# Kernel tuning notes

Measured on AMD Instinct MI355X. Metric: run time of the kernel, lower is better.

## Reference

```python
import jax, jax.numpy as jnp
import numpy as np

D_MODEL = 256
KSIZE = 16
EPS = 1e-5


def conv1d(x, w, b):
    # x: [B, C, N], w: [O, C, K], SAME padding over node axis
    y = jax.lax.conv_general_dilated(x, w, window_strides=(1,), padding='SAME',
                                     dimension_numbers=('NCH', 'OIH', 'NCH'))
    return y + b[None, :, None]


def layernorm(x, g, b):
    mu = jnp.mean(x, axis=-1, keepdims=True)
    var = jnp.mean(jnp.square(x - mu), axis=-1, keepdims=True)
    return (x - mu) * jax.lax.rsqrt(var + EPS) * g + b


def setup_inputs() -> dict:
    key = jax.random.key(0)
    ks = jax.random.split(key, 16)
    B, N, d, K = 4, 2048, D_MODEL, KSIZE
    conv_scale = 1.0 / np.sqrt(d * K)
    lin_scale = 1.0 / np.sqrt(d)
    return {
        'src': jax.random.normal(ks[0], (B, N, d), jnp.float32),
        'x_lst': jnp.zeros((B, N, N), jnp.float32),
        'adj': jax.random.randint(ks[1], (B, N, N), 0, 2, jnp.int32),
        'dis': jax.random.uniform(ks[2], (B, N, N), jnp.float32),
        'Wq': jax.random.normal(ks[3], (d, d, K), jnp.float32) * conv_scale,
        'bq': jnp.zeros((d,), jnp.float32),
        'Wk': jax.random.normal(ks[4], (d, d, K), jnp.float32) * conv_scale,
        'bk': jnp.zeros((d,), jnp.float32),
        'Wv': jax.random.normal(ks[5], (d, d, K), jnp.float32) * conv_scale,
        'bv': jnp.zeros((d,), jnp.float32),
        'W1': jax.random.normal(ks[6], (d, d), jnp.float32) * lin_scale,
        'b1': jnp.zeros((d,), jnp.float32),
        'W2': jax.random.normal(ks[7], (d, d), jnp.float32) * lin_scale,
        'b2': jnp.zeros((d,), jnp.float32),
        'W3': jax.random.normal(ks[8], (d, d), jnp.float32) * lin_scale,
        'b3': jnp.zeros((d,), jnp.float32),
        'g1': jnp.ones((d,), jnp.float32),
        'be1': jnp.zeros((d,), jnp.float32),
        'g2': jnp.ones((d,), jnp.float32),
        'be2': jnp.zeros((d,), jnp.float32),
    }


def reference(src, x_lst, adj, dis, Wq, bq, Wk, bk, Wv, bv,
              W1, b1, W2, b2, W3, b3, g1, be1, g2, be2):
    # ---- _ga_block: transpose to channel-major, graph attention ----
    x = jnp.swapaxes(src, -2, -1)                      # [B, d, N]
    q = conv1d(x, Wq, bq)                              # [B, d, N]
    k = conv1d(x, Wk, bk)
    v = conv1d(x, Wv, bv)
    scale = 1.0 / jnp.sqrt(jnp.asarray(D_MODEL, src.dtype))
    scores = jnp.einsum('bdn,bdm->bnm', q, k) * scale  # [B, N, N]
    scores = scores - dis                              # distance bias
    scores = jnp.where(adj > 0, scores, jnp.asarray(-1e9, scores.dtype))
    attn = jax.nn.softmax(scores, axis=-1)             # [B, N, N]
    x_lst_new = x_lst + attn                           # accumulated attention state
    out = jnp.einsum('bnm,bdm->bdn', attn, v)          # [B, d, N]
    x1 = jnp.swapaxes(out, -2, -1)                     # [B, N, d] (dropout = identity in eval)
    # ---- residual + norm1 ----
    h = layernorm(src + x1, g1, be1)
    # ---- 3-layer LeakyReLU MLP + residual + norm2 ----
    m = jax.nn.leaky_relu(h @ W1.T + b1)
    m = jax.nn.leaky_relu(m @ W2.T + b2)
    m = m @ W3.T + b3
    h = layernorm(h + m, g2, be2)
    return h, x_lst_new
```

## Files before the change

kernel.cpp:

```cpp
#include <hip/hip_runtime.h>
#include <stdint.h>

typedef _Float16 h16;
typedef _Float16 h4v __attribute__((ext_vector_type(4)));
typedef _Float16 h8v __attribute__((ext_vector_type(8)));
typedef float    f4v __attribute__((ext_vector_type(4)));
typedef int      i4v __attribute__((ext_vector_type(4)));

#define NBATCH 4
#define NNODE  2048
#define DM     256
#define NPAD   2063
#define QKELEM 2097152
#define PARTN  (8192 * 256)

__device__ __forceinline__ void async16(const void* g, void* l) {
#if __has_builtin(__builtin_amdgcn_global_load_lds)
  __builtin_amdgcn_global_load_lds((__attribute__((address_space(1))) void*)g,
                                   (__attribute__((address_space(3))) void*)l, 16, 0, 0);
#else
  *(f4v*)l = *(const f4v*)g;
#endif
}

#define BARRIER() do { asm volatile("" ::: "memory"); __builtin_amdgcn_s_barrier(); asm volatile("" ::: "memory"); } while (0)
#define MFMA16 __builtin_amdgcn_mfma_f32_16x16x32_f16

__device__ __forceinline__ void gemm_tile(
    const h16* Abase, int astride,
    const h16* Bbase, int bstride,
    h16* As, h16* Bs, f4v acc[4][4], int kiters)
{
  const int tid  = threadIdx.x;
  const int lane = tid & 63;
  const int wv   = tid >> 6;
  const int srow = tid >> 2;
  const int sch  = ((tid & 3) ^ ((tid >> 3) & 3)) * 8;
  const h16* gA0 = Abase + (long)srow * astride + sch;
  const h16* gA1 = Abase + (long)(srow + 64) * astride + sch;
  const h16* gB0 = Bbase + (long)srow * bstride + sch;
  const h16* gB1 = Bbase + (long)(srow + 64) * bstride + sch;
  h16* lA0 = As + tid * 8;
  h16* lA1 = As + 2048 + tid * 8;
  h16* lB0 = Bs + tid * 8;
  h16* lB1 = Bs + 2048 + tid * 8;
  const int swz = ((lane & 15) >> 1) & 3;
  const int qq  = ((lane >> 4) ^ swz) * 8;
  const int amr = ((wv & 1) * 64 + (lane & 15)) * 32 + qq;
  const int bnr = ((wv >> 1) * 64 + (lane & 15)) * 32 + qq;

  for (int kt = 0; kt < kiters; ++kt) {
    const int k0 = kt * 32;
    __syncthreads();
    async16(gA0 + k0, lA0);
    async16(gA1 + k0, lA1);
    async16(gB0 + k0, lB0);
    async16(gB1 + k0, lB1);
    asm volatile("s_waitcnt vmcnt(0)" ::: "memory");
    __syncthreads();
    h8v af[4], bf[4];
#pragma unroll
    for (int i = 0; i < 4; ++i) af[i] = *(const h8v*)(As + amr + i * 512);
#pragma unroll
    for (int j = 0; j < 4; ++j) bf[j] = *(const h8v*)(Bs + bnr + j * 512);
#pragma unroll
    for (int i = 0; i < 4; ++i)
#pragma unroll
      for (int j = 0; j < 4; ++j)
        acc[i][j] = MFMA16(af[i], bf[j], acc[i][j], 0, 0, 0);
  }
}

__device__ __forceinline__ void zero_acc(f4v acc[4][4]) {
#pragma unroll
  for (int i = 0; i < 4; ++i)
#pragma unroll
    for (int j = 0; j < 4; ++j) {
      f4v z = {0.f, 0.f, 0.f, 0.f};
      acc[i][j] = z;
    }
}

#define NSRC_BLK 8252
__global__ __launch_bounds__(256) void prep_all_kernel(
    const float* __restrict__ src,
    const float* __restrict__ Wq, const float* __restrict__ Wk, const float* __restrict__ Wv,
    const float* __restrict__ W1, const float* __restrict__ W2, const float* __restrict__ W3,
    h16* __restrict__ Xpad, h16* __restrict__ Wt, h16* __restrict__ Wl)
{
  __shared__ float plds[16][257];
  const int bi = blockIdx.x, tid = threadIdx.x;
  if (bi < NSRC_BLK) {
    int idx = bi * 256 + tid;
    int c = idx & 255;
    int row = idx >> 8;
    int b = row / NPAD;
    int n = row - b * NPAD;
    float v = 0.f;
    int ns = n - 7;
    if (ns >= 0 && ns < NNODE) v = src[((long)b * NNODE + ns) * DM + c];
    Xpad[idx] = (h16)v;
  } else if (bi < NSRC_BLK + 768) {
    const int q = bi - NSRC_BLK;
    const int w = q >> 8, o = q & 255;
    const float* W = (w == 0) ? Wq : (w == 1) ? Wk : Wv;
    const float* base = W + (long)o * 4096;
    f4v r0 = *(const f4v*)(base + tid * 16);
    f4v r1 = *(const f4v*)(base + tid * 16 + 4);
    f4v r2 = *(const f4v*)(base + tid * 16 + 8);
    f4v r3 = *(const f4v*)(base + tid * 16 + 12);
#pragma unroll
    for (int k = 0; k < 4; ++k) {
      plds[k][tid] = r0[k]; plds[4 + k][tid] = r1[k];
      plds[8 + k][tid] = r2[k]; plds[12 + k][tid] = r3[k];
    }
    __syncthreads();
    const int t = tid >> 4, c0 = (tid & 15) * 16;
    h16* out = Wt + ((long)(w * 256 + o)) * 4096 + t * 256 + c0;
    h8v o0, o1;
#pragma unroll
    for (int k = 0; k < 8; ++k) { o0[k] = (h16)plds[t][c0 + k]; o1[k] = (h16)plds[t][c0 + 8 + k]; }
    *(h8v*)out = o0;
    *(h8v*)(out + 8) = o1;
  } else {
    int idx = (bi - NSRC_BLK - 768) * 256 + tid;
    int w = idx >> 16;
    int rem = idx & 65535;
    const float* W = (w == 0) ? W1 : (w == 1) ? W2 : W3;
    Wl[idx] = (h16)W[rem];
  }
}

__global__ __launch_bounds__(512) void conv_gemm256_kernel(
    const h16* __restrict__ Xpad, const h16* __restrict__ Wt,
    h16* __restrict__ Qp, h16* __restrict__ Kp, h16* __restrict__ Vp)
{
  __shared__ __align__(16) h16 As[32768];
  __shared__ __align__(16) h16 Bs[32768];
  const int tid  = threadIdx.x;
  const int lane = tid & 63, wv = tid >> 6;
  const int mt = blockIdx.x, w = blockIdx.y, ks = blockIdx.z;
  const int m0 = mt * 256;
  const int b  = m0 >> 11, n0 = m0 & 2047;

  const int rh = tid >> 3;
  const int cs = (((tid & 7) ^ ((tid >> 3) & 7)) << 3);
  const h16* AgT = Xpad + ((long)(b * NPAD + n0) << 8) + ((long)ks << 11) + (long)rh * 256 + cs;
  const h16* BgT = Wt + ((long)w << 20) + ((long)ks << 11) + (long)rh * 4096 + cs;
  h16* lA = As + tid * 8;
  h16* lB = Bs + tid * 8;

  auto stageA = [&](int kt, int half) {
    h16* d = lA + ((kt & 1) << 14) + (half << 13);
    const h16* g = AgT + half * (128 * 256) + kt * 64;
    async16(g, d);
    async16(g + 64 * 256, d + 4096);
  };
  auto stageB = [&](int kt, int half) {
    h16* d = lB + ((kt & 1) << 14) + (half << 13);
    const h16* g = BgT + half * (128 * 4096) + kt * 64;
    async16(g, d);
    async16(g + 64 * 4096, d + 4096);
  };

  const int wr = wv >> 2, wc = wv & 3;
  const int e0 = (((lane >> 4) ^ (lane & 7)) << 3);
  const int e1 = e0 ^ 32;
  const h16* pA0 = As + (wr * 128 + (lane & 15)) * 64 + e0;
  const h16* pA1 = pA0 + (e1 - e0);
  const h16* pB0 = Bs + (wc * 64 + (lane & 15)) * 64 + e0;
  const h16* pB1 = pB0 + (e1 - e0);

  f4v acc[8][4];
#pragma unroll
  for (int i = 0; i < 8; ++i)
#pragma unroll
    for (int j = 0; j < 4; ++j) { f4v z = {0.f, 0.f, 0.f, 0.f}; acc[i][j] = z; }

  stageA(0, 0); stageA(0, 1); stageB(0, 0); stageB(0, 1); stageA(1, 0);
  asm volatile("s_waitcnt vmcnt(2)" ::: "memory");
  BARRIER();

#pragma unroll 1
  for (int kt = 0; kt < 32; ++kt) {
    const int sb = (kt & 1) << 14;
    h8v ar[4][2], bL[2][2], bR[2][2];
#pragma unroll
    for (int i = 0; i < 4; ++i) {
      ar[i][0] = *(const h8v*)(pA0 + sb + i * 1024);
      ar[i][1] = *(const h8v*)(pA1 + sb + i * 1024);
    }
#pragma unroll
    for (int j = 0; j < 2; ++j) {
      bL[j][0] = *(const h8v*)(pB0 + sb + j * 1024);
      bL[j][1] = *(const h8v*)(pB1 + sb + j * 1024);
    }
    if (kt < 31) stageA(kt + 1, 1);
    BARRIER();
    __builtin_amdgcn_s_setprio(1);
#pragma unroll
    for (int i = 0; i < 4; ++i)
#pragma unroll
      for (int j = 0; j < 2; ++j) {
        acc[i][j] = MFMA16(ar[i][0], bL[j][0], acc[i][j], 0, 0, 0);
        acc[i][j] = MFMA16(ar[i][1], bL[j][1], acc[i][j], 0, 0, 0);
      }
    __builtin_amdgcn_s_setprio(0);
    BARRIER();
#pragma unroll
    for (int j = 0; j < 2; ++j) {
      bR[j][0] = *(const h8v*)(pB0 + sb + (j + 2) * 1024);
      bR[j][1] = *(const h8v*)(pB1 + sb + (j + 2) * 1024);
    }
    if (kt < 31) stageB(kt + 1, 0);
    BARRIER();
    __builtin_amdgcn_s_setprio(1);
#pragma unroll
    for (int i = 0; i < 4; ++i)
#pragma unroll
      for (int j = 0; j < 2; ++j) {
        acc[i][j + 2] = MFMA16(ar[i][0], bR[j][0], acc[i][j + 2], 0, 0, 0);
        acc[i][j + 2] = MFMA16(ar[i][1], bR[j][1], acc[i][j + 2], 0, 0, 0);
      }
    __builtin_amdgcn_s_setprio(0);
    BARRIER();
#pragma unroll
    for (int i = 0; i < 4; ++i) {
      ar[i][0] = *(const h8v*)(pA0 + sb + (i + 4) * 1024);
      ar[i][1] = *(const h8v*)(pA1 + sb + (i + 4) * 1024);
    }
    if (kt < 31) stageB(kt + 1, 1);
    BARRIER();
    __builtin_amdgcn_s_setprio(1);
#pragma unroll
    for (int i = 0; i < 4; ++i)
#pragma unroll
      for (int j = 0; j < 2; ++j) {
        acc[i + 4][j + 2] = MFMA16(ar[i][0], bR[j][0], acc[i + 4][j + 2], 0, 0, 0);
        acc[i + 4][j + 2] = MFMA16(ar[i][1], bR[j][1], acc[i + 4][j + 2], 0, 0, 0);
      }
    __builtin_amdgcn_s_setprio(0);
    BARRIER();
#pragma unroll
    for (int j = 0; j < 2; ++j) {
      bL[j][0] = *(const h8v*)(pB0 + sb + j * 1024);
      bL[j][1] = *(const h8v*)(pB1 + sb + j * 1024);
    }
    if (kt < 30) {
      stageA(kt + 2, 0);
      asm volatile("s_waitcnt vmcnt(2)" ::: "memory");
    } else if (kt == 30) {
      asm volatile("s_waitcnt vmcnt(0)" ::: "memory");
    }
    BARRIER();
    __builtin_amdgcn_s_setprio(1);
#pragma unroll
    for (int i = 0; i < 4; ++i)
#pragma unroll
      for (int j = 0; j < 2; ++j) {
        acc[i + 4][j] = MFMA16(ar[i][0], bL[j][0], acc[i + 4][j], 0, 0, 0);
        acc[i + 4][j] = MFMA16(ar[i][1], bL[j][1], acc[i + 4][j], 0, 0, 0);
      }
    __builtin_amdgcn_s_setprio(0);
    BARRIER();
  }

  h16* dst = ((w == 0) ? Qp : (w == 1) ? Kp : Vp) + (long)ks * QKELEM;
  const int rb = (lane >> 4) * 4;
  const int cb = wc * 64 + (lane & 15);
  const int mrow0 = m0 + wr * 128;
#pragma unroll
  for (int i = 0; i < 8; ++i)
#pragma unroll
    for (int j = 0; j < 4; ++j) {
      const int gc = cb + j * 16;
#pragma unroll
      for (int e = 0; e < 4; ++e) {
        const int gr = mrow0 + i * 16 + rb + e;
        dst[(long)gr * 256 + gc] = (h16)acc[i][j][e];
      }
    }
}

__global__ __launch_bounds__(256) void conv_reduce_kernel(
    const h16* __restrict__ Qp, const h16* __restrict__ Kp, const h16* __restrict__ Vp,
    const float* __restrict__ bq, const float* __restrict__ bk, const float* __restrict__ bv,
    h16* __restrict__ Qb, h16* __restrict__ Kb, h16* __restrict__ Vt)
{
  __shared__ float T[64][65];
  const int bi = blockIdx.x, tid = threadIdx.x;
  if (bi < 2048) {
    const long gid = (long)bi * 256 + tid;
    const int which = gid >= (QKELEM / 8);
    const long e = (gid - (long)which * (QKELEM / 8)) * 8;
    const h16* P = which ? Kp : Qp;
    const float* bias = which ? bk : bq;
    h8v p0 = *(const h8v*)(P + e);
    h8v p1 = *(const h8v*)(P + QKELEM + e);
    const int c0 = (int)(e & 255);
    h8v o;
#pragma unroll
    for (int k = 0; k < 8; ++k) o[k] = (h16)((float)p0[k] + (float)p1[k] + bias[c0 + k]);
    *(h8v*)((which ? Kb : Qb) + e) = o;
  } else {
    const int q = bi - 2048;
    const int mt = q >> 2, ct = q & 3;
    const int m0 = mt * 64, c0 = ct * 64;
    const int b = m0 >> 11, n0 = m0 & 2047;
    const int rr = tid >> 3, cc = (tid & 7) * 8;
#pragma unroll
    for (int p = 0; p < 2; ++p) {
      const int r = p * 32 + rr;
      const long so = (long)(m0 + r) * 256 + c0 + cc;
      h8v p0 = *(const h8v*)(Vp + so);
      h8v p1 = *(const h8v*)(Vp + QKELEM + so);
#pragma unroll
      for (int e = 0; e < 8; ++e) T[r][cc + e] = (float)p0[e] + (float)p1[e];
    }
    __syncthreads();
#pragma unroll
    for (int p = 0; p < 2; ++p) {
      const int d = p * 32 + rr;
      const float bias_v = bv[c0 + d];
      h8v o;
#pragma unroll
      for (int e = 0; e < 8; ++e) o[e] = (h16)(T[cc + e][d] + bias_v);
      *(h8v*)(Vt + ((long)(b * 256 + c0 + d)) * 2048 + n0 + cc) = o;
    }
  }
}

__global__ __launch_bounds__(256) void scores_gemm_kernel(
    const h16* __restrict__ Q, const h16* __restrict__ Km, h16* __restrict__ Sh)
{
  __shared__ __align__(16) h16 As[4096];
  __shared__ __align__(16) h16 Bs[4096];
  const int nt = blockIdx.x, mt = blockIdx.y, b = blockIdx.z;
  const h16* Abase = Q + ((long)b * NNODE + nt * 128) * 256;
  const h16* Bbase = Km + ((long)b * NNODE + mt * 128) * 256;
  f4v acc[4][4];
  zero_acc(acc);
  gemm_tile(Abase, 256, Bbase, 256, As, Bs, acc, 8);

  const int lane = threadIdx.x & 63, wv = threadIdx.x >> 6;
  const int rbase = (wv & 1) * 64 + (lane >> 4) * 4;
  const int cbase = (wv >> 1) * 64 + (lane & 15);
  h16* Srow = Sh + (long)b * NNODE * NNODE;
#pragma unroll
  for (int i = 0; i < 4; ++i) {
#pragma unroll
    for (int e = 0; e < 4; ++e) {
      const long row = nt * 128 + rbase + i * 16 + e;
#pragma unroll
      for (int j = 0; j < 4; ++j) {
        const int col = mt * 128 + cbase + j * 16;
        Srow[row * 2048 + col] = (h16)(acc[i][j][e] * 0.0625f);
      }
    }
  }
}

__device__ __forceinline__ float wred_max(float v) {
#pragma unroll
  for (int off = 32; off > 0; off >>= 1) v = fmaxf(v, __shfl_xor(v, off, 64));
  return v;
}
__device__ __forceinline__ float wred_sum(float v) {
#pragma unroll
  for (int off = 32; off > 0; off >>= 1) v += __shfl_xor(v, off, 64);
  return v;
}

__global__ __launch_bounds__(256) void softmax_kernel(
    h16* __restrict__ Sh, const float* __restrict__ dis, const int* __restrict__ adj,
    const float* __restrict__ x_lst, float* __restrict__ out_x)
{
  const int r = blockIdx.x;
  const long ro = (long)r * 2048;
  const int tid = threadIdx.x, lane = tid & 63, wv = tid >> 6;
  const int j0 = tid * 8;
  __shared__ float wmax[4], wsum[4];

  h8v sv = *(const h8v*)(Sh + ro + j0);
  f4v d0 = *(const f4v*)(dis + ro + j0);
  f4v d1 = *(const f4v*)(dis + ro + j0 + 4);
  i4v a0 = *(const i4v*)(adj + ro + j0);
  i4v a1 = *(const i4v*)(adj + ro + j0 + 4);

  float s[8];
#pragma unroll
  for (int k = 0; k < 4; ++k) s[k]     = (a0[k] > 0) ? ((float)sv[k]     - d0[k]) : -1e9f;
#pragma unroll
  for (int k = 0; k < 4; ++k) s[k + 4] = (a1[k] > 0) ? ((float)sv[k + 4] - d1[k]) : -1e9f;

  float m = s[0];
#pragma unroll
  for (int k = 1; k < 8; ++k) m = fmaxf(m, s[k]);
  m = wred_max(m);
  if (lane == 0) wmax[wv] = m;
  __syncthreads();
  m = fmaxf(fmaxf(wmax[0], wmax[1]), fmaxf(wmax[2], wmax[3]));

  float p[8], ls = 0.f;
#pragma unroll
  for (int k = 0; k < 8; ++k) { p[k] = __expf(s[k] - m); ls += p[k]; }
  ls = wred_sum(ls);
  if (lane == 0) wsum[wv] = ls;
  __syncthreads();
  const float inv = 1.0f / (wsum[0] + wsum[1] + wsum[2] + wsum[3]);

  f4v x0 = *(const f4v*)(x_lst + ro + j0);
  f4v x1 = *(const f4v*)(x_lst + ro + j0 + 4);
  f4v o0, o1;
  h8v pv;
#pragma unroll
  for (int k = 0; k < 4; ++k) {
    const float a = p[k] * inv, bq = p[k + 4] * inv;
    o0[k] = x0[k] + a; o1[k] = x1[k] + bq;
    pv[k] = (h16)a; pv[k + 4] = (h16)bq;
  }
  *(f4v*)(out_x + ro + j0) = o0;
  *(f4v*)(out_x + ro + j0 + 4) = o1;
  *(h8v*)(Sh + ro + j0) = pv;
}

__global__ __launch_bounds__(256) void av_gemm_kernel(
    const h16* __restrict__ Attn, const h16* __restrict__ Vt, h16* __restrict__ X1p)
{
  __shared__ __align__(16) h16 As[4096];
  __shared__ __align__(16) h16 Bs[4096];
  const int nt = blockIdx.x, b = blockIdx.z;
  const int ct = blockIdx.y & 1, ks = blockIdx.y >> 1;
  const h16* Abase = Attn + ((long)b * NNODE + nt * 128) * 2048 + ks * 1024;
  const h16* Bbase = Vt + ((long)b * 256 + ct * 128) * 2048 + ks * 1024;
  f4v acc[4][4];
  zero_acc(acc);
  gemm_tile(Abase, 2048, Bbase, 2048, As, Bs, acc, 32);

  const int lane = threadIdx.x & 63, wv = threadIdx.x >> 6;
  const int rbase = (wv & 1) * 64 + (lane >> 4) * 4;
  const int cbase = (wv >> 1) * 64 + (lane & 15);
  h16* dst = X1p + (long)ks * PARTN;
#pragma unroll
  for (int i = 0; i < 4; ++i) {
#pragma unroll
    for (int e = 0; e < 4; ++e) {
      const long row = (long)b * NNODE + nt * 128 + rbase + i * 16 + e;
#pragma unroll
      for (int j = 0; j < 4; ++j) {
        const int col = ct * 128 + cbase + j * 16;
        dst[row * 256 + col] = (h16)acc[i][j][e];
      }
    }
  }
}

__global__ __launch_bounds__(256) void ln1_kernel(
    const float* __restrict__ X, const h16* __restrict__ Y, const h16* __restrict__ Y2,
    const float* __restrict__ g, const float* __restrict__ bb,
    float* __restrict__ outF, h16* __restrict__ outH)
{
  const int wv = threadIdx.x >> 6, lane = threadIdx.x & 63;
  const long r = (long)blockIdx.x * 4 + wv;
  const long off = r * 256 + lane * 4;
  f4v x = *(const f4v*)(X + off);
  h4v y = *(const h4v*)(Y + off);
  h4v y2 = *(const h4v*)(Y2 + off);
  float v[4];
  float sum = 0.f, sq = 0.f;
#pragma unroll
  for (int k = 0; k < 4; ++k) {
    v[k] = x[k] + (float)y[k] + (float)y2[k];
    sum += v[k]; sq += v[k] * v[k];
  }
  sum = wred_sum(sum);
  sq  = wred_sum(sq);
  const float mu = sum * (1.0f / 256.0f);
  const float var = sq * (1.0f / 256.0f) - mu * mu;
  const float rs = rsqrtf(var + 1e-5f);
  f4v gg = *(const f4v*)(g + lane * 4);
  f4v be = *(const f4v*)(bb + lane * 4);
  f4v o;
#pragma unroll
  for (int k = 0; k < 4; ++k) o[k] = (v[k] - mu) * rs * gg[k] + be[k];
  *(f4v*)(outF + off) = o;
  h4v hv;
#pragma unroll
  for (int k = 0; k < 4; ++k) hv[k] = (h16)o[k];
  *(h4v*)(outH + off) = hv;
}

__global__ __launch_bounds__(256) void mlp_fused_kernel(
    const h16* __restrict__ H16, const float* __restrict__ Hf,
    const h16* __restrict__ Wl,
    const float* __restrict__ b1, const float* __restrict__ b2, const float* __restrict__ b3,
    const float* __restrict__ g2, const float* __restrict__ be2,
    float* __restrict__ out_h)
{
  __shared__ h16 Xa[32][264];
  __shared__ h16 Xb[32][264];
  __shared__ __align__(16) h16 Bs[8192];
  const int tid = threadIdx.x, lane = tid & 63, wv = tid >> 6;
  const int m0 = blockIdx.x * 32;

  {
    const int r = tid >> 3, cq = (tid & 7) * 32;
    const h16* s = H16 + (long)(m0 + r) * 256 + cq;
#pragma unroll
    for (int k = 0; k < 4; ++k)
      *(h8v*)&Xa[r][cq + k * 8] = *(const h8v*)(s + k * 8);
  }

  const int srow = tid >> 2;
  const int sch  = ((tid & 3) ^ ((tid >> 3) & 3)) * 8;
  h16* lB = Bs + tid * 8;
  const int quad = lane >> 4;
  const float* biases[3] = {b1, b2, b3};

  for (int layer = 0; layer < 3; ++layer) {
    const h16* W = Wl + layer * 65536;
    const h16 (*Xi)[264] = (layer == 1) ? (const h16(*)[264])Xb : (const h16(*)[264])Xa;
    h16 (*Xo)[264] = (layer == 1) ? Xa : Xb;
    f4v acc[2][4];
#pragma unroll
    for (int i = 0; i < 2; ++i)
#pragma unroll
      for (int j = 0; j < 4; ++j) { f4v z = {0.f,0.f,0.f,0.f}; acc[i][j] = z; }

    for (int kt = 0; kt < 8; ++kt) {
      __syncthreads();
      const h16* gB = W + (long)srow * 256 + kt * 32 + sch;
      async16(gB, lB);
      async16(gB + 64 * 256, lB + 64 * 32);
      async16(gB + 128 * 256, lB + 128 * 32);
      async16(gB + 192 * 256, lB + 192 * 32);
      asm volatile("s_waitcnt vmcnt(0)" ::: "memory");
      __syncthreads();
      h8v af[2], bf[4];
#pragma unroll
      for (int i = 0; i < 2; ++i)
        af[i] = *(const h8v*)&Xi[i * 16 + (lane & 15)][kt * 32 + quad * 8];
#pragma unroll
      for (int j = 0; j < 4; ++j) {
        const int n = wv * 64 + j * 16 + (lane & 15);
        const int q = (quad ^ ((n >> 1) & 3)) * 8;
        bf[j] = *(const h8v*)(Bs + n * 32 + q);
      }
#pragma unroll
      for (int i = 0; i < 2; ++i)
#pragma unroll
        for (int j = 0; j < 4; ++j)
          acc[i][j] = MFMA16(af[i], bf[j], acc[i][j], 0, 0, 0);
    }
    const int rb = quad * 4;
    const int cb = wv * 64 + (lane & 15);
    const float* bias = biases[layer];
    const bool leaky = (layer < 2);
#pragma unroll
    for (int j = 0; j < 4; ++j) {
      const int col = cb + j * 16;
      const float bv = bias[col];
#pragma unroll
      for (int i = 0; i < 2; ++i)
#pragma unroll
        for (int e = 0; e < 4; ++e) {
          float v = acc[i][j][e] + bv;
          if (leaky) v = (v >= 0.f) ? v : 0.01f * v;
          Xo[i * 16 + rb + e][col] = (h16)v;
        }
    }
  }
  __syncthreads();

  const int r = tid >> 3, c0 = (tid & 7) * 32;
  const float* hrow = Hf + (long)(m0 + r) * 256 + c0;
  float v[32];
  float s = 0.f, sq = 0.f;
#pragma unroll
  for (int k8 = 0; k8 < 8; ++k8) {
    f4v h4 = *(const f4v*)(hrow + k8 * 4);
#pragma unroll
    for (int e = 0; e < 4; ++e) {
      float t = (float)Xb[r][c0 + k8 * 4 + e] + h4[e];
      v[k8 * 4 + e] = t; s += t; sq += t * t;
    }
  }
#pragma unroll
  for (int off = 1; off < 8; off <<= 1) { s += __shfl_xor(s, off, 64); sq += __shfl_xor(sq, off, 64); }
  const float mu = s * (1.0f / 256.0f);
  const float var = sq * (1.0f / 256.0f) - mu * mu;
  const float rs = rsqrtf(var + 1e-5f);
  float* orow = out_h + (long)(m0 + r) * 256 + c0;
#pragma unroll
  for (int k8 = 0; k8 < 8; ++k8) {
    f4v gg = *(const f4v*)(g2 + c0 + k8 * 4);
    f4v be = *(const f4v*)(be2 + c0 + k8 * 4);
    f4v o;
#pragma unroll
    for (int e = 0; e < 4; ++e) o[e] = (v[k8 * 4 + e] - mu) * rs * gg[e] + be[e];
    *(f4v*)(orow + k8 * 4) = o;
  }
}

extern "C" void kernel_launch(void* const* d_in, const int* in_sizes, int n_in,
                              void* d_out, int out_size, void* d_ws, size_t ws_size,
                              hipStream_t stream)
{
  const float* src  = (const float*)d_in[0];
  const float* xlst = (const float*)d_in[1];
  const int*   adj  = (const int*)d_in[2];
  const float* dis  = (const float*)d_in[3];
  const float* Wq   = (const float*)d_in[4];
  const float* bq   = (const float*)d_in[5];
  const float* Wk   = (const float*)d_in[6];
  const float* bk   = (const float*)d_in[7];
  const float* Wv   = (const float*)d_in[8];
  const float* bvp  = (const float*)d_in[9];
  const float* W1   = (const float*)d_in[10];
  const float* b1   = (const float*)d_in[11];
  const float* W2   = (const float*)d_in[12];
  const float* b2   = (const float*)d_in[13];
  const float* W3   = (const float*)d_in[14];
  const float* b3   = (const float*)d_in[15];
  const float* g1   = (const float*)d_in[16];
  const float* be1  = (const float*)d_in[17];
  const float* g2   = (const float*)d_in[18];
  const float* be2  = (const float*)d_in[19];
  (void)in_sizes; (void)n_in; (void)out_size; (void)ws_size;

  char* ws = (char*)d_ws;
  size_t off = 0;
  auto alloc = [&](size_t bytes) -> void* {
    void* p = ws + off;
    off += (bytes + 1023) & ~(size_t)1023;
    return p;
  };
  h16*   Xpad = (h16*)  alloc((size_t)NBATCH * NPAD * DM * 2);
  h16*   Wt   = (h16*)  alloc((size_t)3 * 256 * 4096 * 2);
  h16*   Wl   = (h16*)  alloc((size_t)3 * 256 * 256 * 2);
  h16*   Qb   = (h16*)  alloc((size_t)QKELEM * 2);
  h16*   Kb   = (h16*)  alloc((size_t)QKELEM * 2);
  h16*   Vt   = (h16*)  alloc((size_t)QKELEM * 2);
  char*  R    = (char*) alloc((size_t)66000 * 1024);
  h16*   Qp   = (h16*)R;
  h16*   Kp   = (h16*)(R + (size_t)2 * QKELEM * 2);
  h16*   Vp   = (h16*)(R + (size_t)4 * QKELEM * 2);
  h16*   Sh   = (h16*)R;
  h16*   X1p  = (h16*)(R + (size_t)8 * QKELEM * 2);
  float* H    = (float*)(R + (size_t)12 * QKELEM * 2);
  h16*   H16  = (h16*)((char*)H + (size_t)PARTN * 4);

  float* out_h = (float*)d_out;
  float* out_x = out_h + (size_t)NBATCH * NNODE * DM;

  prep_all_kernel<<<NSRC_BLK + 768 + 768, 256, 0, stream>>>(
      src, Wq, Wk, Wv, W1, W2, W3, Xpad, Wt, Wl);
  conv_gemm256_kernel<<<dim3(32, 3, 2), 512, 0, stream>>>(Xpad, Wt, Qp, Kp, Vp);
  conv_reduce_kernel<<<2048 + 512, 256, 0, stream>>>(
      Qp, Kp, Vp, bq, bk, bvp, Qb, Kb, Vt);
  scores_gemm_kernel<<<dim3(16, 16, 4), 256, 0, stream>>>(Qb, Kb, Sh);
  softmax_kernel<<<NBATCH * NNODE, 256, 0, stream>>>(Sh, dis, adj, xlst, out_x);
  av_gemm_kernel<<<dim3(16, 4, 4), 256, 0, stream>>>(Sh, Vt, X1p);
  ln1_kernel<<<(NBATCH * NNODE) / 4, 256, 0, stream>>>(src, X1p, X1p + PARTN, g1, be1, H, H16);
  mlp_fused_kernel<<<NBATCH * NNODE / 32, 256, 0, stream>>>(
      H16, H, Wl, b1, b2, b3, g2, be2, out_h);
}
```

Baseline: 417.8 us.

## Use 256x256 pipelined tiles for scores GEMM and wave-per-row softmax

Factors the double-buffered 256x256 MFMA pipeline out of the conv GEMM into a reusable template. It then applies that template to the QK^T scores GEMM, replacing 128x128 tiles with larger 512-thread blocks to raise operand reuse. Softmax now processes one row per wavefront, with 32 values per lane, removing shared-memory reductions and block barriers. The trade-offs are fewer blocks in the scores GEMM, which may underfill the GPU given the short K loop, and higher register pressure in softmax.

```diff
diff --git a/kernel.cpp b/kernel.cpp
--- a/kernel.cpp
+++ b/kernel.cpp
@@ -79,6 +79,136 @@
       f4v z = {0.f, 0.f, 0.f, 0.f};
       acc[i][j] = z;
     }
+}
+
+template<int ASTRIDE, int BSTRIDE>
+__device__ __forceinline__ void gemm256_pipe(
+    const h16* __restrict__ Abase, const h16* __restrict__ Bbase,
+    h16* As, h16* Bs, f4v (&acc)[8][4], const int kiters)
+{
+  const int tid  = threadIdx.x;
+  const int lane = tid & 63, wv = tid >> 6;
+
+  const int rh = tid >> 3;
+  const int cs = (((tid & 7) ^ ((tid >> 3) & 7)) << 3);
+  const h16* AgT = Abase + (long)rh * ASTRIDE + cs;
+  const h16* BgT = Bbase + (long)rh * BSTRIDE + cs;
+  h16* lA = As + tid * 8;
+  h16* lB = Bs + tid * 8;
+
+  auto stageA = [&](int kt, int half) {
+    h16* d = lA + ((kt & 1) << 14) + (half << 13);
+    const h16* g = AgT + (long)half * 128 * ASTRIDE + kt * 64;
+    async16(g, d);
+    async16(g + 64 * ASTRIDE, d + 4096);
+  };
+  auto stageB = [&](int kt, int half) {
+    h16* d = lB + ((kt & 1) << 14) + (half << 13);
+    const h16* g = BgT + (long)half * 128 * BSTRIDE + kt * 64;
+    async16(g, d);
+    async16(g + 64 * BSTRIDE, d + 4096);
+  };
+
+  const int wr = wv >> 2, wc = wv & 3;
+  const int e0 = (((lane >> 4) ^ (lane & 7)) << 3);
+  const int e1 = e0 ^ 32;
+  const h16* pA0 = As + (wr * 128 + (lane & 15)) * 64 + e0;
+  const h16* pA1 = pA0 + (e1 - e0);
+  const h16* pB0 = Bs + (wc * 64 + (lane & 15)) * 64 + e0;
+  const h16* pB1 = pB0 + (e1 - e0);
+
+#pragma unroll
+  for (int i = 0; i < 8; ++i)
+#pragma unroll
+    for (int j = 0; j < 4; ++j) { f4v z = {0.f, 0.f, 0.f, 0.f}; acc[i][j] = z; }
+
+  stageA(0, 0); stageA(0, 1); stageB(0, 0); stageB(0, 1); stageA(1, 0);
+  asm volatile("s_waitcnt vmcnt(2)" ::: "memory");
+  BARRIER();
+
+#pragma unroll 1
+  for (int kt = 0; kt < kiters; ++kt) {
+    const int sb = (kt & 1) << 14;
+    h8v ar[4][2], bL[2][2], bR[2][2];
+#pragma unroll
+    for (int i = 0; i < 4; ++i) {
+      ar[i][0] = *(const h8v*)(pA0 + sb + i * 1024);
+      ar[i][1] = *(const h8v*)(pA1 + sb + i * 1024);
+    }
+#pragma unroll
+    for (int j = 0; j < 2; ++j) {
+      bL[j][0] = *(const h8v*)(pB0 + sb + j * 1024);
+      bL[j][1] = *(const h8v*)(pB1 + sb + j * 1024);
+    }
+    if (kt < kiters - 1) stageA(kt + 1, 1);
+    BARRIER();
+    __builtin_amdgcn_s_setprio(1);
+#pragma unroll
+    for (int i = 0; i < 4; ++i)
+#pragma unroll
+      for (int j = 0; j < 2; ++j) {
+        acc[i][j] = MFMA16(ar[i][0], bL[j][0], acc[i][j], 0, 0, 0);
+        acc[i][j] = MFMA16(ar[i][1], bL[j][1], acc[i][j], 0, 0, 0);
+      }
+    __builtin_amdgcn_s_setprio(0);
+    BARRIER();
+#pragma unroll
+    for (int j = 0; j < 2; ++j) {
+      bR[j][0] = *(const h8v*)(pB0 + sb + (j + 2) * 1024);
+      bR[j][1] = *(const h8v*)(pB1 + sb + (j + 2) * 1024);
+    }
+    if (kt < kiters - 1) stageB(kt + 1, 0);
+    BARRIER();
+    __builtin_amdgcn_s_setprio(1);
+#pragma unroll
+    for (int i = 0; i < 4; ++i)
+#pragma unroll
+      for (int j = 0; j < 2; ++j) {
+        acc[i][j + 2] = MFMA16(ar[i][0], bR[j][0], acc[i][j + 2], 0, 0, 0);
+        acc[i][j + 2] = MFMA16(ar[i][1], bR[j][1], acc[i][j + 2], 0, 0, 0);
+      }
+    __builtin_amdgcn_s_setprio(0);
+    BARRIER();
+#pragma unroll
+    for (int i = 0; i < 4; ++i) {
+      ar[i][0] = *(const h8v*)(pA0 + sb + (i + 4) * 1024);
+      ar[i][1] = *(const h8v*)(pA1 + sb + (i + 4) * 1024);
+    }
+    if (kt < kiters - 1) stageB(kt + 1, 1);
+    BARRIER();
+    __builtin_amdgcn_s_setprio(1);
+#pragma unroll
+    for (int i = 0; i < 4; ++i)
+#pragma unroll
+      for (int j = 0; j < 2; ++j) {
+        acc[i + 4][j + 2] = MFMA16(ar[i][0], bR[j][0], acc[i + 4][j + 2], 0, 0, 0);
+        acc[i + 4][j + 2] = MFMA16(ar[i][1], bR[j][1], acc[i + 4][j + 2], 0, 0, 0);
+      }
+    __builtin_amdgcn_s_setprio(0);
+    BARRIER();
+#pragma unroll
+    for (int j = 0; j < 2; ++j) {
+      bL[j][0] = *(const h8v*)(pB0 + sb + j * 1024);
+      bL[j][1] = *(const h8v*)(pB1 + sb + j * 1024);
+    }
+    if (kt < kiters - 2) {
+      stageA(kt + 2, 0);
+      asm volatile("s_waitcnt vmcnt(2)" ::: "memory");
+    } else if (kt == kiters - 2) {
+      asm volatile("s_waitcnt vmcnt(0)" ::: "memory");
+    }
+    BARRIER();
+    __builtin_amdgcn_s_setprio(1);
+#pragma unroll
+    for (int i = 0; i < 4; ++i)
+#pragma unroll
+      for (int j = 0; j < 2; ++j) {
+        acc[i + 4][j] = MFMA16(ar[i][0], bL[j][0], acc[i + 4][j], 0, 0, 0);
+        acc[i + 4][j] = MFMA16(ar[i][1], bL[j][1], acc[i + 4][j], 0, 0, 0);
+      }
+    __builtin_amdgcn_s_setprio(0);
+    BARRIER();
+  }
 }
 
 #define NSRC_BLK 8252
@@ -137,135 +267,19 @@
 {
   __shared__ __align__(16) h16 As[32768];
   __shared__ __align__(16) h16 Bs[32768];
-  const int tid  = threadIdx.x;
-  const int lane = tid & 63, wv = tid >> 6;
+  const int lane = threadIdx.x & 63, wv = threadIdx.x >> 6;
   const int mt = blockIdx.x, w = blockIdx.y, ks = blockIdx.z;
   const int m0 = mt * 256;
   const int b  = m0 >> 11, n0 = m0 & 2047;
 
-  const int rh = tid >> 3;
-  const int cs = (((tid & 7) ^ ((tid >> 3) & 7)) << 3);
-  const h16* AgT = Xpad + ((long)(b * NPAD + n0) << 8) + ((long)ks << 11) + (long)rh * 256 + cs;
-  const h16* BgT = Wt + ((long)w << 20) + ((long)ks << 11) + (long)rh * 4096 + cs;
-  h16* lA = As + tid * 8;
-  h16* lB = Bs + tid * 8;
-
-  auto stageA = [&](int kt, int half) {
-    h16* d = lA + ((kt & 1) << 14) + (half << 13);
-    const h16* g = AgT + half * (128 * 256) + kt * 64;
-    async16(g, d);
-    async16(g + 64 * 256, d + 4096);
-  };
-  auto stageB = [&](int kt, int half) {
-    h16* d = lB + ((kt & 1) << 14) + (half << 13);
-    const h16* g = BgT + half * (128 * 4096) + kt * 64;
-    async16(g, d);
-    async16(g + 64 * 4096, d + 4096);
-  };
-
+  const h16* Abase = Xpad + ((long)(b * NPAD + n0) << 8) + ((long)ks << 11);
+  const h16* Bbase = Wt + ((long)w << 20) + ((long)ks << 11);
+
+  f4v acc[8][4];
+  gemm256_pipe<256, 4096>(Abase, Bbase, As, Bs, acc, 32);
+
+  h16* dst = ((w == 0) ? Qp : (w == 1) ? Kp : Vp) + (long)ks * QKELEM;
   const int wr = wv >> 2, wc = wv & 3;
-  const int e0 = (((lane >> 4) ^ (lane & 7)) << 3);
-  const int e1 = e0 ^ 32;
-  const h16* pA0 = As + (wr * 128 + (lane & 15)) * 64 + e0;
-  const h16* pA1 = pA0 + (e1 - e0);
-  const h16* pB0 = Bs + (wc * 64 + (lane & 15)) * 64 + e0;
-  const h16* pB1 = pB0 + (e1 - e0);
-
-  f4v acc[8][4];
-#pragma unroll
-  for (int i = 0; i < 8; ++i)
-#pragma unroll
-    for (int j = 0; j < 4; ++j) { f4v z = {0.f, 0.f, 0.f, 0.f}; acc[i][j] = z; }
-
-  stageA(0, 0); stageA(0, 1); stageB(0, 0); stageB(0, 1); stageA(1, 0);
-  asm volatile("s_waitcnt vmcnt(2)" ::: "memory");
-  BARRIER();
-
-#pragma unroll 1
-  for (int kt = 0; kt < 32; ++kt) {
-    const int sb = (kt & 1) << 14;
-    h8v ar[4][2], bL[2][2], bR[2][2];
-#pragma unroll
-    for (int i = 0; i < 4; ++i) {
-      ar[i][0] = *(const h8v*)(pA0 + sb + i * 1024);
-      ar[i][1] = *(const h8v*)(pA1 + sb + i * 1024);
-    }
-#pragma unroll
-    for (int j = 0; j < 2; ++j) {
-      bL[j][0] = *(const h8v*)(pB0 + sb + j * 1024);
-      bL[j][1] = *(const h8v*)(pB1 + sb + j * 1024);
-    }
-    if (kt < 31) stageA(kt + 1, 1);
-    BARRIER();
-    __builtin_amdgcn_s_setprio(1);
-#pragma unroll
-    for (int i = 0; i < 4; ++i)
-#pragma unroll
-      for (int j = 0; j < 2; ++j) {
-        acc[i][j] = MFMA16(ar[i][0], bL[j][0], acc[i][j], 0, 0, 0);
-        acc[i][j] = MFMA16(ar[i][1], bL[j][1], acc[i][j], 0, 0, 0);
-      }
-    __builtin_amdgcn_s_setprio(0);
-    BARRIER();
-#pragma unroll
-    for (int j = 0; j < 2; ++j) {
-      bR[j][0] = *(const h8v*)(pB0 + sb + (j + 2) * 1024);
-      bR[j][1] = *(const h8v*)(pB1 + sb + (j + 2) * 1024);
-    }
-    if (kt < 31) stageB(kt + 1, 0);
-    BARRIER();
-    __builtin_amdgcn_s_setprio(1);
-#pragma unroll
-    for (int i = 0; i < 4; ++i)
-#pragma unroll
-      for (int j = 0; j < 2; ++j) {
-        acc[i][j + 2] = MFMA16(ar[i][0], bR[j][0], acc[i][j + 2], 0, 0, 0);
-        acc[i][j + 2] = MFMA16(ar[i][1], bR[j][1], acc[i][j + 2], 0, 0, 0);
-      }
-    __builtin_amdgcn_s_setprio(0);
-    BARRIER();
-#pragma unroll
-    for (int i = 0; i < 4; ++i) {
-      ar[i][0] = *(const h8v*)(pA0 + sb + (i + 4) * 1024);
-      ar[i][1] = *(const h8v*)(pA1 + sb + (i + 4) * 1024);
-    }
-    if (kt < 31) stageB(kt + 1, 1);
-    BARRIER();
-    __builtin_amdgcn_s_setprio(1);
-#pragma unroll
-    for (int i = 0; i < 4; ++i)
-#pragma unroll
-      for (int j = 0; j < 2; ++j) {
-        acc[i + 4][j + 2] = MFMA16(ar[i][0], bR[j][0], acc[i + 4][j + 2], 0, 0, 0);
-        acc[i + 4][j + 2] = MFMA16(ar[i][1], bR[j][1], acc[i + 4][j + 2], 0, 0, 0);
-      }
-    __builtin_amdgcn_s_setprio(0);
-    BARRIER();
-#pragma unroll
-    for (int j = 0; j < 2; ++j) {
-      bL[j][0] = *(const h8v*)(pB0 + sb + j * 1024);
-      bL[j][1] = *(const h8v*)(pB1 + sb + j * 1024);
-    }
-    if (kt < 30) {
-      stageA(kt + 2, 0);
-      asm volatile("s_waitcnt vmcnt(2)" ::: "memory");
-    } else if (kt == 30) {
-      asm volatile("s_waitcnt vmcnt(0)" ::: "memory");
-    }
-    BARRIER();
-    __builtin_amdgcn_s_setprio(1);
-#pragma unroll
-    for (int i = 0; i < 4; ++i)
-#pragma unroll
-      for (int j = 0; j < 2; ++j) {
-        acc[i + 4][j] = MFMA16(ar[i][0], bL[j][0], acc[i + 4][j], 0, 0, 0);
-        acc[i + 4][j] = MFMA16(ar[i][1], bL[j][1], acc[i + 4][j], 0, 0, 0);
-      }
-    __builtin_amdgcn_s_setprio(0);
-    BARRIER();
-  }
-
-  h16* dst = ((w == 0) ? Qp : (w == 1) ? Kp : Vp) + (long)ks * QKELEM;
   const int rb = (lane >> 4) * 4;
   const int cb = wc * 64 + (lane & 15);
   const int mrow0 = m0 + wr * 128;
@@ -330,98 +344,96 @@
   }
 }
 
-__global__ __launch_bounds__(256) void scores_gemm_kernel(
+__global__ __launch_bounds__(512) void scores_gemm256_kernel(
     const h16* __restrict__ Q, const h16* __restrict__ Km, h16* __restrict__ Sh)
 {
-  __shared__ __align__(16) h16 As[4096];
-  __shared__ __align__(16) h16 Bs[4096];
+  __shared__ __align__(16) h16 As[32768];
+  __shared__ __align__(16) h16 Bs[32768];
+  const int lane = threadIdx.x & 63, wv = threadIdx.x >> 6;
   const int nt = blockIdx.x, mt = blockIdx.y, b = blockIdx.z;
-  const h16* Abase = Q + ((long)b * NNODE + nt * 128) * 256;
-  const h16* Bbase = Km + ((long)b * NNODE + mt * 128) * 256;
-  f4v acc[4][4];
-  zero_acc(acc);
-  gemm_tile(Abase, 256, Bbase, 256, As, Bs, acc, 8);
-
-  const int lane = threadIdx.x & 63, wv = threadIdx.x >> 6;
-  const int rbase = (wv & 1) * 64 + (lane >> 4) * 4;
-  const int cbase = (wv >> 1) * 64 + (lane & 15);
+
+  const h16* Abase = Q + ((long)b * NNODE + nt * 256) * 256;
+  const h16* Bbase = Km + ((long)b * NNODE + mt * 256) * 256;
+
+  f4v acc[8][4];
+  gemm256_pipe<256, 256>(Abase, Bbase, As, Bs, acc, 4);
+
+  const int wr = wv >> 2, wc = wv & 3;
+  const int rb = (lane >> 4) * 4;
+  const int cb = wc * 64 + (lane & 15);
   h16* Srow = Sh + (long)b * NNODE * NNODE;
-#pragma unroll
-  for (int i = 0; i < 4; ++i) {
+  const int row0 = nt * 256 + wr * 128;
+  const int col0 = mt * 256;
+#pragma unroll
+  for (int i = 0; i < 8; ++i) {
 #pragma unroll
     for (int e = 0; e < 4; ++e) {
-      const long row = nt * 128 + rbase + i * 16 + e;
+      const long row = row0 + i * 16 + rb + e;
 #pragma unroll
       for (int j = 0; j < 4; ++j) {
-        const int col = mt * 128 + cbase + j * 16;
+        const int col = col0 + cb + j * 16;
         Srow[row * 2048 + col] = (h16)(acc[i][j][e] * 0.0625f);
       }
     }
   }
-}
-
-__device__ __forceinline__ float wred_max(float v) {
-#pragma unroll
-  for (int off = 32; off > 0; off >>= 1) v = fmaxf(v, __shfl_xor(v, off, 64));
-  return v;
-}
-__device__ __forceinline__ float wred_sum(float v) {
-#pragma unroll
-  for (int off = 32; off > 0; off >>= 1) v += __shfl_xor(v, off, 64);
-  return v;
 }
 
 __global__ __launch_bounds__(256) void softmax_kernel(
     h16* __restrict__ Sh, const float* __restrict__ dis, const int* __restrict__ adj,
     const float* __restrict__ x_lst, float* __restrict__ out_x)
 {
-  const int r = blockIdx.x;
-  const long ro = (long)r * 2048;
-  const int tid = threadIdx.x, lane = tid & 63, wv = tid >> 6;
-  const int j0 = tid * 8;
-  __shared__ float wmax[4], wsum[4];
-
-  h8v sv = *(const h8v*)(Sh + ro + j0);
-  f4v d0 = *(const f4v*)(dis + ro + j0);
-  f4v d1 = *(const f4v*)(dis + ro + j0 + 4);
-  i4v a0 = *(const i4v*)(adj + ro + j0);
-  i4v a1 = *(const i4v*)(adj + ro + j0 + 4);
-
-  float s[8];
-#pragma unroll
-  for (int k = 0; k < 4; ++k) s[k]     = (a0[k] > 0) ? ((float)sv[k]     - d0[k]) : -1e9f;
-#pragma unroll
-  for (int k = 0; k < 4; ++k) s[k + 4] = (a1[k] > 0) ? ((float)sv[k + 4] - d1[k]) : -1e9f;
-
-  float m = s[0];
-#pragma unroll
-  for (int k = 1; k < 8; ++k) m = fmaxf(m, s[k]);
-  m = wred_max(m);
-  if (lane == 0) wmax[wv] = m;
-  __syncthreads();
-  m = fmaxf(fmaxf(wmax[0], wmax[1]), fmaxf(wmax[2], wmax[3]));
-
-  float p[8], ls = 0.f;
-#pragma unroll
-  for (int k = 0; k < 8; ++k) { p[k] = __expf(s[k] - m); ls += p[k]; }
-  ls = wred_sum(ls);
-  if (lane == 0) wsum[wv] = ls;
-  __syncthreads();
-  const float inv = 1.0f / (wsum[0] + wsum[1] + wsum[2] + wsum[3]);
-
-  f4v x0 = *(const f4v*)(x_lst + ro + j0);
-  f4v x1 = *(const f4v*)(x_lst + ro + j0 + 4);
-  f4v o0, o1;
-  h8v pv;
-#pragma unroll
-  for (int k = 0; k < 4; ++k) {
-    const float a = p[k] * inv, bq = p[k + 4] * inv;
-    o0[k] = x0[k] + a; o1[k] = x1[k] + bq;
-    pv[k] = (h16)a; pv[k + 4] = (h16)bq;
-  }
-  *(f4v*)(out_x + ro + j0) = o0;
-  *(f4v*)(out_x + ro + j0 + 4) = o1;
-  *(h8v*)(Sh + ro + j0) = pv;
+  const int wv = threadIdx.x >> 6, lane = threadIdx.x & 63;
+  const long r = (long)blockIdx.x * 4 + wv;
+  const long ro = r * 2048;
+  const int j0 = lane * 8;
+
+  h8v sv[4];
+#pragma unroll
+  for (int c = 0; c < 4; ++c) sv[c] = *(const h8v*)(Sh + ro + c * 512 + j0);
+
+  float s[32];
+  float m = -3e38f;
+#pragma unroll
+  for (int c = 0; c < 4; ++c) {
+    f4v d0 = *(const f4v*)(dis + ro + c * 512 + j0);
+    f4v d1 = *(const f4v*)(dis + ro + c * 512 + j0 + 4);
+    i4v a0 = *(const i4v*)(adj + ro + c * 512 + j0);
+    i4v a1 = *(const i4v*)(adj + ro + c * 512 + j0 + 4);
+#pragma unroll
+    for (int k = 0; k < 4; ++k) {
+      const float t0 = (a0[k] > 0) ? ((float)sv[c][k] - d0[k]) : -1e9f;
+      const float t1 = (a1[k] > 0) ? ((float)sv[c][k + 4] - d1[k]) : -1e9f;
+      s[c * 8 + k] = t0;
+      s[c * 8 + 4 + k] = t1;
+      m = fmaxf(m, fmaxf(t0, t1));
+    }
+  }
+#pragma unroll
+  for (int off = 32; off > 0; off >>= 1) m = fmaxf(m, __shfl_xor(m, off, 64));
+
+  float ls = 0.f;
+#pragma unroll
+  for (int k = 0; k < 32; ++k) { s[k] = __expf(s[k] - m); ls += s[k]; }
+#pragma unroll
+  for (int off = 32; off > 0; off >>= 1) ls += __shfl_xor(ls, off, 64);
+  const float inv = 1.0f / ls;
+
+#pragma unroll
+  for (int c = 0; c < 4; ++c) {
+    f4v x0 = *(const f4v*)(x_lst + ro + c * 512 + j0);
+    f4v x1 = *(const f4v*)(x_lst + ro + c * 512 + j0 + 4);
+    f4v o0, o1;
+    h8v pv;
+#pragma unroll
+    for (int k = 0; k < 4; ++k) {
+      const float pa = s[c * 8 + k] * inv, pb = s[c * 8 + 4 + k] * inv;
+      o0[k] = x0[k] + pa; o1[k] = x1[k] + pb;
+      pv[k] = (h16)pa; pv[k + 4] = (h16)pb;
+    }
+    *(f4v*)(out_x + ro + c * 512 + j0) = o0;
+    *(f4v*)(out_x + ro + c * 512 + j0 + 4) = o1;
+    *(h8v*)(Sh + ro + c * 512 + j0) = pv;
+  }
 }
 
 __global__ __launch_bounds__(256) void av_gemm_kernel(
@@ -453,6 +465,12 @@
       }
     }
   }
+}
+
+__device__ __forceinline__ float wred_sum(float v) {
+#pragma unroll
+  for (int off = 32; off > 0; off >>= 1) v += __shfl_xor(v, off, 64);
+  return v;
 }
 
 __global__ __launch_bounds__(256) void ln1_kernel(
@@ -658,8 +676,8 @@
   conv_gemm256_kernel<<<dim3(32, 3, 2), 512, 0, stream>>>(Xpad, Wt, Qp, Kp, Vp);
   conv_reduce_kernel<<<2048 + 512, 256, 0, stream>>>(
       Qp, Kp, Vp, bq, bk, bvp, Qb, Kb, Vt);
-  scores_gemm_kernel<<<dim3(16, 16, 4), 256, 0, stream>>>(Qb, Kb, Sh);
-  softmax_kernel<<<NBATCH * NNODE, 256, 0, stream>>>(Sh, dis, adj, xlst, out_x);
+  scores_gemm256_kernel<<<dim3(8, 8, 4), 512, 0, stream>>>(Qb, Kb, Sh);
+  softmax_kernel<<<NBATCH * NNODE / 4, 256, 0, stream>>>(Sh, dis, adj, xlst, out_x);
   av_gemm_kernel<<<dim3(16, 4, 4), 256, 0, stream>>>(Sh, Vt, X1p);
   ln1_kernel<<<(NBATCH * NNODE) / 4, 256, 0, stream>>>(src, X1p, X1p + PARTN, g1, be1, H, H16);
   mlp_fused_kernel<<<NBATCH * NNODE / 32, 256, 0, stream>>>(
```

Result: no change. 424.7 us (+1.6%).
